# Kernel optimization log

Hardware: AMD Instinct MI355X
Metric: run time of the kernel (lower is better)

Reference implementation:

```python
import jax, jax.numpy as jnp
import numpy as np

NEG = -1e9  # finite mask value (avoids NaN rows for fully-masked queries)


def setup_inputs() -> dict:
    key = jax.random.key(0)
    kq, kk, kv, ks = jax.random.split(key, 4)
    B, H, N, E = 4, 8, 2048, 64
    Q = jax.random.normal(kq, (B, H, N, E), dtype=jnp.float32)
    K = jax.random.normal(kk, (B, H, N, E), dtype=jnp.float32)
    V = jax.random.normal(kv, (B, H, N, E), dtype=jnp.float32)
    seqlens = jax.random.randint(ks, (B,), 1, N + 1, dtype=jnp.int32)
    return {"Q": Q, "K": K, "V": V, "seqlens": seqlens}


def reference(Q, K, V, seqlens):
    # SparTA SeqlenDynamicSparseAttention: per-batch masked attention.
    # scores = Q @ K^T (no 1/sqrt(E) scaling inside the kernel; Q/K are
    # assumed to be already-projected), softmax over keys < seqlen[b],
    # output zeroed for query rows >= seqlen[b].
    B, H, N, E = Q.shape
    pos = jnp.arange(N)
    valid = pos[None, :] < seqlens[:, None]  # [B, N] bool
    scores = jnp.einsum('bhqe,bhke->bhqk', Q, K)  # [B,H,N,N]
    scores = jnp.where(valid[:, None, None, :], scores, NEG)
    probs = jax.nn.softmax(scores, axis=-1)
    out = jnp.einsum('bhqk,bhke->bhqe', probs, V)  # [B,H,N,E]
    out = jnp.where(valid[:, None, :, None], out, 0.0)
    return out
```

## Files before the change

kernel.cpp:

```cpp
#include <hip/hip_runtime.h>

using f32x4  = __attribute__((ext_vector_type(4))) float;
using f32x16 = __attribute__((ext_vector_type(16))) float;
using h16x2  = __attribute__((ext_vector_type(2))) _Float16;
using h16x4  = __attribute__((ext_vector_type(4))) _Float16;
using h16x8  = __attribute__((ext_vector_type(8))) _Float16;
using fp16x2 = __attribute__((ext_vector_type(2))) __fp16;

#define NEGBIG (-1e30f)
#define LOG2E  1.44269504f

constexpr int BH = 32, Nn = 2048, En = 64;

__device__ inline h16x8 cvt8(f32x4 x, f32x4 y) {
    union { h16x8 v; fp16x2 p[4]; } u;
    u.p[0] = __builtin_amdgcn_cvt_pkrtz(x[0], x[1]);
    u.p[1] = __builtin_amdgcn_cvt_pkrtz(x[2], x[3]);
    u.p[2] = __builtin_amdgcn_cvt_pkrtz(y[0], y[1]);
    u.p[3] = __builtin_amdgcn_cvt_pkrtz(y[2], y[3]);
    return u.v;
}
__device__ inline h16x4 cvt4(f32x4 x) {
    union { h16x4 v; fp16x2 p[2]; } u;
    u.p[0] = __builtin_amdgcn_cvt_pkrtz(x[0], x[1]);
    u.p[1] = __builtin_amdgcn_cvt_pkrtz(x[2], x[3]);
    return u.v;
}
__device__ inline fp16x2 shfl32(fp16x2 x) {
    union { fp16x2 h; int i; } u; u.h = x;
    u.i = __shfl_xor(u.i, 32);
    return u.h;
}

#define TILE_BARRIER() asm volatile("s_waitcnt lgkmcnt(0)\ns_barrier" ::: "memory")

__launch_bounds__(256, 3)
__global__ void attn_part(const float* __restrict__ Qg,
                          const float* __restrict__ Kg,
                          const float* __restrict__ Vg,
                          const int*   __restrict__ seqlens,
                          _Float16*    __restrict__ Opart,
                          float*       __restrict__ Wpart,
                          int chunk)
{
    const int qblk = blockIdx.x;
    const int bh   = blockIdx.y;
    const int s    = blockIdx.z;
    const int seqlen = seqlens[bh >> 3];
    const int qstart = qblk * 128;
    const int kbeg   = s * chunk;
    if (qstart >= seqlen || kbeg >= seqlen) return;
    const int kend = min(seqlen, kbeg + chunk);

    const float* Qb = Qg + (size_t)bh * Nn * En;
    const float* Kb = Kg + (size_t)bh * Nn * En;
    const float* Vb = Vg + (size_t)bh * Nn * En;
    const int tid = threadIdx.x;

    __shared__ __attribute__((aligned(16))) _Float16 Ksh[2][64 * 64];
    __shared__ __attribute__((aligned(16))) _Float16 Vsh[2][64 * 64];

    const int wid  = tid >> 6;
    const int lane = tid & 63;
    const int l31  = lane & 31;
    const int h    = lane >> 5;

    const int qbase = qstart + wid * 32;
    const bool active = qbase < seqlen;
    const int qrow = qbase + l31;

    h16x8 Qf[4];
    #pragma unroll
    for (int es = 0; es < 4; ++es) {
        const f32x4* qp = (const f32x4*)(Qb + (size_t)qrow * En + es * 16 + h * 8);
        f32x4 x = qp[0] * LOG2E, y = qp[1] * LOG2E;
        Qf[es] = cvt8(x, y);
    }

    const int vkey = tid & 63;
    const int vw   = tid >> 6;

    const f32x16 z16 = {0,0,0,0,0,0,0,0,0,0,0,0,0,0,0,0};
    float m = NEGBIG, L = 0.f;
    f32x16 Ot[2] = {z16, z16};

    f32x4 kr[2][2], vr[2][2];

    auto loadStage = [&](int ks) {
        #pragma unroll
        for (int it = 0; it < 2; ++it) {
            int cid = tid + 256 * it;
            int r = cid >> 3, c = cid & 7;
            const f32x4* kp = (const f32x4*)(Kb + (size_t)(ks + r) * En + c * 8);
            kr[it][0] = kp[0]; kr[it][1] = kp[1];
            const f32x4* vp = (const f32x4*)(Vb + (size_t)(ks + vkey) * En + vw * 8 + 32 * it);
            vr[it][0] = vp[0]; vr[it][1] = vp[1];
        }
    };

    auto writeStage = [&](int db) {
        #pragma unroll
        for (int it = 0; it < 2; ++it) {
            int cid = tid + 256 * it;
            int r = cid >> 3, c = cid & 7;
            *(h16x8*)&Ksh[db][r * 64 + ((c ^ (r & 7)) << 3)] = cvt8(kr[it][0], kr[it][1]);
            int e0 = vw * 8 + 32 * it;
            float vv[8] = {vr[it][0][0], vr[it][0][1], vr[it][0][2], vr[it][0][3],
                           vr[it][1][0], vr[it][1][1], vr[it][1][2], vr[it][1][3]};
            #pragma unroll
            for (int i = 0; i < 8; ++i) {
                int e = e0 + i;
                Vsh[db][e * 64 + (((vkey >> 2) ^ (i << 1)) << 2) + (vkey & 3)] =
                    (_Float16)vv[i];
            }
        }
    };

    auto computeTile = [&](int db, int ks) {
        if (!active) return;
        const _Float16* Kl = Ksh[db];
        const _Float16* Vl = Vsh[db];

        f32x16 St[2];
        #pragma unroll
        for (int kt = 0; kt < 2; ++kt) {
            f32x16 acc = z16;
            #pragma unroll
            for (int es = 0; es < 4; ++es) {
                h16x8 kf = *(const h16x8*)
                    &Kl[(32 * kt + l31) * 64 + ((((es << 1) + h) ^ (l31 & 7)) << 3)];
                acc = __builtin_amdgcn_mfma_f32_32x32x16_f16(kf, Qf[es], acc, 0, 0, 0);
            }
            St[kt] = acc;
        }
        if (ks + 64 > seqlen) {
            #pragma unroll
            for (int kt = 0; kt < 2; ++kt) {
                #pragma unroll
                for (int r = 0; r < 16; ++r) {
                    int key = ks + 32 * kt + 4 * h + ((r & 3) + 8 * (r >> 2));
                    if (key >= seqlen) St[kt][r] = NEGBIG;
                }
            }
        }

        float tm = St[0][0];
        #pragma unroll
        for (int r = 1; r < 16; ++r) tm = fmaxf(tm, St[0][r]);
        #pragma unroll
        for (int r = 0; r < 16; ++r) tm = fmaxf(tm, St[1][r]);
        tm = fmaxf(tm, __shfl_xor(tm, 32));

        if (__any(tm > m + 8.f)) {
            float mn = fmaxf(m, tm);
            float sc = __builtin_amdgcn_exp2f(m - mn);
            m = mn; L *= sc;
            Ot[0] *= sc; Ot[1] *= sc;
        }

        float ps = 0.f;
        fp16x2 pk[2][8];
        #pragma unroll
        for (int kt = 0; kt < 2; ++kt) {
            #pragma unroll
            for (int mm = 0; mm < 8; ++mm) {
                float p0 = __builtin_amdgcn_exp2f(St[kt][2 * mm]     - m);
                float p1 = __builtin_amdgcn_exp2f(St[kt][2 * mm + 1] - m);
                ps += p0 + p1;
                pk[kt][mm] = __builtin_amdgcn_cvt_pkrtz(p0, p1);
            }
        }
        ps += __shfl_xor(ps, 32);
        L += ps;

        #pragma unroll
        for (int kstep = 0; kstep < 4; ++kstep) {
            const int kt = kstep >> 1, k4 = (kstep & 1) * 4;
            fp16x2 sendA = h ? pk[kt][k4 + 0] : pk[kt][k4 + 2];
            fp16x2 sendB = h ? pk[kt][k4 + 1] : pk[kt][k4 + 3];
            fp16x2 recvA = shfl32(sendA);
            fp16x2 recvB = shfl32(sendB);
            fp16x2 ownLo = h ? pk[kt][k4 + 2] : pk[kt][k4 + 0];
            fp16x2 ownHi = h ? pk[kt][k4 + 3] : pk[kt][k4 + 1];
            union { h16x8 v; fp16x2 d[4]; } pf;
            pf.d[0] = h ? recvA : ownLo;
            pf.d[1] = h ? recvB : ownHi;
            pf.d[2] = h ? ownLo : recvA;
            pf.d[3] = h ? ownHi : recvB;
            #pragma unroll
            for (int et = 0; et < 2; ++et) {
                h16x8 vf = *(const h16x8*)
                    &Vl[(32 * et + l31) * 64 +
                        ((((kstep << 2) + (h << 1)) ^ ((l31 & 7) << 1)) << 2)];
                Ot[et] = __builtin_amdgcn_mfma_f32_32x32x16_f16(vf, pf.v, Ot[et], 0, 0, 0);
            }
        }
    };

    int ks = kbeg, db = 0;
    loadStage(ks);
    while (true) {
        writeStage(db);
        if (ks + 64 < kend) loadStage(ks + 64);
        TILE_BARRIER();
        computeTile(db, ks);
        ks += 64;
        if (ks >= kend) break;
        db ^= 1;
    }

    if (active && qrow < seqlen) {
        float lw = m + __log2f(L);
        const size_t rbase = ((size_t)s * BH + bh) * Nn + qrow;
        if (h == 0) Wpart[rbase] = lw;
        float invL = 1.f / L;
        _Float16* op = Opart + rbase * En;
        #pragma unroll
        for (int et = 0; et < 2; ++et) {
            #pragma unroll
            for (int r1 = 0; r1 < 4; ++r1) {
                f32x4 o = {Ot[et][4 * r1 + 0] * invL, Ot[et][4 * r1 + 1] * invL,
                           Ot[et][4 * r1 + 2] * invL, Ot[et][4 * r1 + 3] * invL};
                *(h16x4*)&op[et * 32 + r1 * 8 + h * 4] = cvt4(o);
            }
        }
    }
}

__launch_bounds__(256)
__global__ void reduce_k(const _Float16* __restrict__ Opart,
                         const float*    __restrict__ Wpart,
                         const int*      __restrict__ seqlens,
                         float*          __restrict__ Og,
                         int cshift)
{
    const int tid  = threadIdx.x;
    const int r    = tid >> 3;
    const int e8   = tid & 7;
    const int grow = blockIdx.x * 32 + r;
    const int bh   = grow >> 11;
    const int row  = grow & (Nn - 1);
    const int seqlen = seqlens[bh >> 3];

    f32x4 a0 = {0, 0, 0, 0}, a1 = {0, 0, 0, 0};
    if (row < seqlen) {
        const int chunk = 1 << cshift;
        const int nlive = (seqlen + chunk - 1) >> cshift;
        float W = NEGBIG;
        for (int s = 0; s < nlive; ++s)
            W = fmaxf(W, Wpart[((size_t)s * BH + bh) * Nn + row]);
        float denom = 0.f;
        for (int s = 0; s < nlive; ++s) {
            const size_t rbase = ((size_t)s * BH + bh) * Nn + row;
            float a = __builtin_amdgcn_exp2f(Wpart[rbase] - W);
            denom += a;
            h16x8 o = *(const h16x8*)&Opart[rbase * En + e8 * 8];
            a0[0] += a * (float)o[0]; a0[1] += a * (float)o[1];
            a0[2] += a * (float)o[2]; a0[3] += a * (float)o[3];
            a1[0] += a * (float)o[4]; a1[1] += a * (float)o[5];
            a1[2] += a * (float)o[6]; a1[3] += a * (float)o[7];
        }
        float sc = 1.f / denom;
        a0 *= sc; a1 *= sc;
    }
    float* op = Og + ((size_t)bh * Nn + row) * En + e8 * 8;
    *(f32x4*)op       = a0;
    *(f32x4*)(op + 4) = a1;
}

__launch_bounds__(512)
__global__ void attn_kernel(const float* __restrict__ Qg,
                            const float* __restrict__ Kg,
                            const float* __restrict__ Vg,
                            const int*   __restrict__ seqlens,
                            float*       __restrict__ Og)
{
    const int qblk = blockIdx.x;
    const int bh   = blockIdx.y;
    const int seqlen = seqlens[bh >> 3];
    const int qstart = qblk * 128;
    const int tid = threadIdx.x;
    float* Ob = Og + ((size_t)bh * Nn + qstart) * En;
    if (qstart >= seqlen) {
        f32x4 z = {0.f, 0.f, 0.f, 0.f};
        f32x4* op = (f32x4*)Ob;
        #pragma unroll
        for (int i = 0; i < 4; ++i) op[tid + i * 512] = z;
        return;
    }
    const float* Qb = Qg + (size_t)bh * Nn * En;
    const float* Kb = Kg + (size_t)bh * Nn * En;
    const float* Vb = Vg + (size_t)bh * Nn * En;
    __shared__ __attribute__((aligned(16))) _Float16 Ksh[64 * 64];
    __shared__ __attribute__((aligned(16))) _Float16 Vsh[64 * 64];
    const int wid  = tid >> 6;
    const int qsub = wid >> 2;
    const int widq = wid & 3;
    const int lane = tid & 63;
    const int lg   = lane >> 4;
    const int l16  = lane & 15;
    const bool active = (qstart + qsub * 64) < seqlen;
    const int qrow = qstart + qsub * 64 + widq * 16 + l16;
    h16x8 Qf[2];
    #pragma unroll
    for (int es = 0; es < 2; ++es) {
        const f32x4* qp = (const f32x4*)(Qb + (size_t)qrow * En + es * 32 + lg * 8);
        f32x4 x = qp[0] * LOG2E, y = qp[1] * LOG2E;
        Qf[es] = cvt8(x, y);
    }
    const int rK = tid >> 3, cK = tid & 7, vkey = tid & 63, ve0 = (tid >> 6) * 8;
    float m = NEGBIG, L = 0.f;
    f32x4 Ot[4] = {{0,0,0,0},{0,0,0,0},{0,0,0,0},{0,0,0,0}};
    auto loadStage = [&](int ks, f32x4& k0, f32x4& k1, f32x4& v0, f32x4& v1) {
        const f32x4* kp = (const f32x4*)(Kb + (size_t)(ks + rK) * En + cK * 8);
        k0 = kp[0]; k1 = kp[1];
        const f32x4* vp = (const f32x4*)(Vb + (size_t)(ks + vkey) * En + ve0);
        v0 = vp[0]; v1 = vp[1];
    };
    auto writeStage = [&](const f32x4& k0, const f32x4& k1,
                          const f32x4& v0, const f32x4& v1) {
        *(h16x8*)&Ksh[rK * 64 + ((cK ^ (rK & 7)) << 3)] = cvt8(k0, k1);
        float vv[8] = {v0[0], v0[1], v0[2], v0[3], v1[0], v1[1], v1[2], v1[3]};
        #pragma unroll
        for (int i = 0; i < 8; ++i) {
            int e = ve0 + i;
            Vsh[e * 64 + (((vkey >> 2) ^ (i << 1)) << 2) + (vkey & 3)] =
                (_Float16)vv[i];
        }
    };
    auto computeTile = [&](int ks) {
        if (!active) return;
        f32x4 St[4];
        #pragma unroll
        for (int kt = 0; kt < 4; ++kt) {
            f32x4 acc = {0, 0, 0, 0};
            int key = kt * 16 + l16;
            #pragma unroll
            for (int es = 0; es < 2; ++es) {
                int c = es * 4 + lg;
                h16x8 kf = *(const h16x8*)&Ksh[key * 64 + ((c ^ (key & 7)) << 3)];
                acc = __builtin_amdgcn_mfma_f32_16x16x32_f16(kf, Qf[es], acc, 0, 0, 0);
            }
            St[kt] = acc;
        }
        if (ks + 64 > seqlen) {
            #pragma unroll
            for (int kt = 0; kt < 4; ++kt) {
                int kb0 = ks + kt * 16 + lg * 4;
                #pragma unroll
                for (int j = 0; j < 4; ++j)
                    if (kb0 + j >= seqlen) St[kt][j] = NEGBIG;
            }
        }
        float tm = NEGBIG;
        #pragma unroll
        for (int kt = 0; kt < 4; ++kt)
            #pragma unroll
            for (int j = 0; j < 4; ++j) tm = fmaxf(tm, St[kt][j]);
        tm = fmaxf(tm, __shfl_xor(tm, 16));
        tm = fmaxf(tm, __shfl_xor(tm, 32));
        if (__any(tm > m + 8.f)) {
            float mn = fmaxf(m, tm);
            float sc = __builtin_amdgcn_exp2f(m - mn);
            m = mn; L *= sc;
            #pragma unroll
            for (int et = 0; et < 4; ++et) Ot[et] *= sc;
        }
        float ps = 0.f;
        h16x4 Pf[4];
        #pragma unroll
        for (int kt = 0; kt < 4; ++kt) {
            float p0 = __builtin_amdgcn_exp2f(St[kt][0] - m);
            float p1 = __builtin_amdgcn_exp2f(St[kt][1] - m);
            float p2 = __builtin_amdgcn_exp2f(St[kt][2] - m);
            float p3 = __builtin_amdgcn_exp2f(St[kt][3] - m);
            ps += (p0 + p1) + (p2 + p3);
            union { h16x4 v; fp16x2 p[2]; } u;
            u.p[0] = __builtin_amdgcn_cvt_pkrtz(p0, p1);
            u.p[1] = __builtin_amdgcn_cvt_pkrtz(p2, p3);
            Pf[kt] = u.v;
        }
        ps += __shfl_xor(ps, 16);
        ps += __shfl_xor(ps, 32);
        L += ps;
        #pragma unroll
        for (int kt = 0; kt < 4; ++kt) {
            #pragma unroll
            for (int et = 0; et < 4; ++et) {
                int e  = et * 16 + l16;
                int c8 = kt * 4 + lg;
                h16x4 vf = *(const h16x4*)&Vsh[e * 64 + ((c8 ^ ((e & 7) << 1)) << 2)];
                Ot[et] = __builtin_amdgcn_mfma_f32_16x16x16f16(vf, Pf[kt], Ot[et], 0, 0, 0);
            }
        }
    };
    f32x4 kA0, kA1, vA0, vA1, kB0, kB1, vB0, vB1;
    loadStage(0, kA0, kA1, vA0, vA1);
    int ks = 0;
    while (true) {
        __syncthreads();
        writeStage(kA0, kA1, vA0, vA1);
        if (ks + 64 < seqlen) loadStage(ks + 64, kB0, kB1, vB0, vB1);
        __syncthreads();
        computeTile(ks);
        ks += 64;
        if (ks >= seqlen) break;
        __syncthreads();
        writeStage(kB0, kB1, vB0, vB1);
        if (ks + 64 < seqlen) loadStage(ks + 64, kA0, kA1, vA0, vA1);
        __syncthreads();
        computeTile(ks);
        ks += 64;
        if (ks >= seqlen) break;
    }
    float invL = 1.f / L;
    float* orow = Ob + (size_t)(qsub * 64 + widq * 16 + l16) * En;
    if (qrow < seqlen) {
        #pragma unroll
        for (int et = 0; et < 4; ++et) {
            f32x4 o = Ot[et] * invL;
            *(f32x4*)(orow + et * 16 + lg * 4) = o;
        }
    } else {
        f32x4 z = {0, 0, 0, 0};
        #pragma unroll
        for (int et = 0; et < 4; ++et)
            *(f32x4*)(orow + et * 16 + lg * 4) = z;
    }
}

extern "C" void kernel_launch(void* const* d_in, const int* in_sizes, int n_in,
                              void* d_out, int out_size, void* d_ws, size_t ws_size,
                              hipStream_t stream)
{
    const float* Q  = (const float*)d_in[0];
    const float* K  = (const float*)d_in[1];
    const float* V  = (const float*)d_in[2];
    const int*   SL = (const int*)d_in[3];
    float*       O  = (float*)d_out;

    auto need = [](int S) {
        return (size_t)S * BH * Nn * En * sizeof(_Float16)
             + (size_t)S * BH * Nn * sizeof(float);
    };
    int S = 0;
    if      (ws_size >= need(4)) S = 4;
    else if (ws_size >= need(2)) S = 2;

    if (S) {
        _Float16* Opart = (_Float16*)d_ws;
        float*    Wpart = (float*)((char*)d_ws
                            + (size_t)S * BH * Nn * En * sizeof(_Float16));
        const int chunk  = Nn / S;
        const int cshift = (S == 4) ? 9 : 10;
        attn_part<<<dim3(Nn / 128, BH, S), 256, 0, stream>>>(
            Q, K, V, SL, Opart, Wpart, chunk);
        reduce_k<<<dim3(BH * Nn / 32), 256, 0, stream>>>(
            Opart, Wpart, SL, O, cshift);
    } else {
        attn_kernel<<<dim3(Nn / 128, BH), 512, 0, stream>>>(Q, K, V, SL, O);
    }
}
```

Baseline: 132.6 us.

## Single-buffer LDS tiles, raise occupancy target, and allow 8-way key split

Drops the LDS double buffer for K/V and adds an extra barrier before each tile write, halving shared memory per block. Launch bounds go from 3 to 5 blocks per CU so more blocks can be resident. The row-max reduction becomes a tree reduction, and the split-K path can use 8 chunks when the workspace is large enough, which gives more blocks for short sequences. The costs are less overlap between loading and computing, tighter register limits that may cause spills, and more partial results for the reduce kernel to combine.

```diff
diff --git a/kernel.cpp b/kernel.cpp
--- a/kernel.cpp
+++ b/kernel.cpp
@@ -34,7 +34,7 @@
 
 #define TILE_BARRIER() asm volatile("s_waitcnt lgkmcnt(0)\ns_barrier" ::: "memory")
 
-__launch_bounds__(256, 3)
+__launch_bounds__(256, 5)
 __global__ void attn_part(const float* __restrict__ Qg,
                           const float* __restrict__ Kg,
                           const float* __restrict__ Vg,
@@ -57,8 +57,8 @@
     const float* Vb = Vg + (size_t)bh * Nn * En;
     const int tid = threadIdx.x;
 
-    __shared__ __attribute__((aligned(16))) _Float16 Ksh[2][64 * 64];
-    __shared__ __attribute__((aligned(16))) _Float16 Vsh[2][64 * 64];
+    __shared__ __attribute__((aligned(16))) _Float16 Ksh[64 * 64];
+    __shared__ __attribute__((aligned(16))) _Float16 Vsh[64 * 64];
 
     const int wid  = tid >> 6;
     const int lane = tid & 63;
@@ -98,28 +98,26 @@
         }
     };
 
-    auto writeStage = [&](int db) {
+    auto writeStage = [&]() {
         #pragma unroll
         for (int it = 0; it < 2; ++it) {
             int cid = tid + 256 * it;
             int r = cid >> 3, c = cid & 7;
-            *(h16x8*)&Ksh[db][r * 64 + ((c ^ (r & 7)) << 3)] = cvt8(kr[it][0], kr[it][1]);
+            *(h16x8*)&Ksh[r * 64 + ((c ^ (r & 7)) << 3)] = cvt8(kr[it][0], kr[it][1]);
             int e0 = vw * 8 + 32 * it;
             float vv[8] = {vr[it][0][0], vr[it][0][1], vr[it][0][2], vr[it][0][3],
                            vr[it][1][0], vr[it][1][1], vr[it][1][2], vr[it][1][3]};
             #pragma unroll
             for (int i = 0; i < 8; ++i) {
                 int e = e0 + i;
-                Vsh[db][e * 64 + (((vkey >> 2) ^ (i << 1)) << 2) + (vkey & 3)] =
+                Vsh[e * 64 + (((vkey >> 2) ^ (i << 1)) << 2) + (vkey & 3)] =
                     (_Float16)vv[i];
             }
         }
     };
 
-    auto computeTile = [&](int db, int ks) {
+    auto computeTile = [&](int ks) {
         if (!active) return;
-        const _Float16* Kl = Ksh[db];
-        const _Float16* Vl = Vsh[db];
 
         f32x16 St[2];
         #pragma unroll
@@ -128,7 +126,7 @@
             #pragma unroll
             for (int es = 0; es < 4; ++es) {
                 h16x8 kf = *(const h16x8*)
-                    &Kl[(32 * kt + l31) * 64 + ((((es << 1) + h) ^ (l31 & 7)) << 3)];
+                    &Ksh[(32 * kt + l31) * 64 + ((((es << 1) + h) ^ (l31 & 7)) << 3)];
                 acc = __builtin_amdgcn_mfma_f32_32x32x16_f16(kf, Qf[es], acc, 0, 0, 0);
             }
             St[kt] = acc;
@@ -144,12 +142,15 @@
             }
         }
 
-        float tm = St[0][0];
-        #pragma unroll
-        for (int r = 1; r < 16; ++r) tm = fmaxf(tm, St[0][r]);
-        #pragma unroll
-        for (int r = 0; r < 16; ++r) tm = fmaxf(tm, St[1][r]);
-        tm = fmaxf(tm, __shfl_xor(tm, 32));
+        float t[16];
+        #pragma unroll
+        for (int r = 0; r < 16; ++r) t[r] = fmaxf(St[0][r], St[1][r]);
+        #pragma unroll
+        for (int off = 8; off > 0; off >>= 1)
+            #pragma unroll
+            for (int r = 0; r < 8; ++r)
+                if (r < off) t[r] = fmaxf(t[r], t[r + off]);
+        float tm = fmaxf(t[0], __shfl_xor(t[0], 32));
 
         if (__any(tm > m + 8.f)) {
             float mn = fmaxf(m, tm);
@@ -190,23 +191,23 @@
             #pragma unroll
             for (int et = 0; et < 2; ++et) {
                 h16x8 vf = *(const h16x8*)
-                    &Vl[(32 * et + l31) * 64 +
-                        ((((kstep << 2) + (h << 1)) ^ ((l31 & 7) << 1)) << 2)];
+                    &Vsh[(32 * et + l31) * 64 +
+                         ((((kstep << 2) + (h << 1)) ^ ((l31 & 7) << 1)) << 2)];
                 Ot[et] = __builtin_amdgcn_mfma_f32_32x32x16_f16(vf, pf.v, Ot[et], 0, 0, 0);
             }
         }
     };
 
-    int ks = kbeg, db = 0;
+    int ks = kbeg;
     loadStage(ks);
     while (true) {
-        writeStage(db);
+        TILE_BARRIER();
+        writeStage();
         if (ks + 64 < kend) loadStage(ks + 64);
         TILE_BARRIER();
-        computeTile(db, ks);
+        computeTile(ks);
         ks += 64;
         if (ks >= kend) break;
-        db ^= 1;
     }
 
     if (active && qrow < seqlen) {
@@ -443,18 +444,17 @@
         return (size_t)S * BH * Nn * En * sizeof(_Float16)
              + (size_t)S * BH * Nn * sizeof(float);
     };
-    int S = 0;
-    if      (ws_size >= need(4)) S = 4;
-    else if (ws_size >= need(2)) S = 2;
+    int S = 0, cshift = 0;
+    if      (ws_size >= need(8)) { S = 8; cshift = 8;  }
+    else if (ws_size >= need(4)) { S = 4; cshift = 9;  }
+    else if (ws_size >= need(2)) { S = 2; cshift = 10; }
 
     if (S) {
         _Float16* Opart = (_Float16*)d_ws;
         float*    Wpart = (float*)((char*)d_ws
                             + (size_t)S * BH * Nn * En * sizeof(_Float16));
-        const int chunk  = Nn / S;
-        const int cshift = (S == 4) ? 9 : 10;
         attn_part<<<dim3(Nn / 128, BH, S), 256, 0, stream>>>(
-            Q, K, V, SL, Opart, Wpart, chunk);
+            Q, K, V, SL, Opart, Wpart, Nn / S);
         reduce_k<<<dim3(BH * Nn / 32), 256, 0, stream>>>(
             Opart, Wpart, SL, O, cshift);
     } else {
```

Result: slower. 239.7 us (+80.8%).
